# Performance work log

Measured on AMD Instinct MI355X. Metric: run time of the kernel, lower is better.

## Reference

```python
import jax, jax.numpy as jnp
import numpy as np

B, H, S, D = 2, 8, 2048, 64


def setup_inputs() -> dict:
    key = jax.random.key(0)
    kq, kk, kv, km = jax.random.split(key, 4)
    Q = jax.random.normal(kq, (B, H, S, D), dtype=jnp.float32)
    K = jax.random.normal(kk, (B, H, S, D), dtype=jnp.float32)
    V = jax.random.normal(kv, (B, H, S, D), dtype=jnp.float32)
    attn_mask = jax.random.randint(km, (B, H, S, S), 0, 2).astype(jnp.bool_)
    return {"Q": Q, "K": K, "V": V, "attn_mask": attn_mask}


def reference(Q, K, V, attn_mask):
    # a = Q K^T / sqrt(D)
    scale = 1.0 / jnp.sqrt(jnp.float32(Q.shape[-1]))
    a = jnp.einsum("bhqd,bhkd->bhqk", Q, K) * scale
    a = jnp.where(attn_mask, jnp.float32(-1e9), a)
    attn_p = jax.nn.softmax(a, axis=-1)
    # FAITHFUL to source bug: uses pre-softmax scores `a`, not attn_p
    attn_v = jnp.einsum("bhqk,bhkd->bhqd", a, V)
    return attn_v, attn_p
```

## Files before the change

kernel.cpp:

```cpp
#include <hip/hip_runtime.h>
#include <hip/hip_bf16.h>


#define SS   2048
#define DD   64
#define NT   8
#define ZMB  0
#define ZKB  4224
#define ZVB  12928
#define ZRZ  23168
#define ZAH  23296
#define MASK_B 0
#define K_B    4224
#define ARENA_H 8960
#define KST 68
#define FST 132

#define OV_F4 524288
#define ZB_F4 8192
#define PK_OFF  131072
#define PK_BYTES ((size_t)16*2048*16*16)

typedef _Float16 half4_t  __attribute__((ext_vector_type(4)));
typedef _Float16 half2_t  __attribute__((ext_vector_type(2)));
typedef short    short4_t __attribute__((ext_vector_type(4)));
typedef float    float4_t __attribute__((ext_vector_type(4)));
typedef int      int2_t   __attribute__((ext_vector_type(2)));
typedef unsigned uint2_t  __attribute__((ext_vector_type(2)));
typedef unsigned long long ulong2_t __attribute__((ext_vector_type(2)));

static __device__ __forceinline__ unsigned short f2bf_u(float f) {
  __hip_bfloat16 h = __float2bfloat16(f);
  return __builtin_bit_cast(unsigned short, h);
}
static __device__ __forceinline__ unsigned packh2(float a, float b) {
  union { half2_t h; unsigned u; } c;
  c.h.x = (_Float16)a; c.h.y = (_Float16)b;
  return c.u;
}

extern "C" __global__ __launch_bounds__(256)
void zero_k(float4_t* __restrict__ Ov, float4_t* __restrict__ Zb)
{
  const int i = blockIdx.x * 256 + threadIdx.x;
  const float4_t z = (float4_t){0.f, 0.f, 0.f, 0.f};
  if (i < OV_F4) Ov[i] = z;
  else           Zb[i - OV_F4] = z;
}

extern "C" __global__ __launch_bounds__(256, 1)
void attn_z_k(const float* __restrict__ Qg, const float* __restrict__ Kg,
              const float* __restrict__ Vg, const int* __restrict__ Mg,
              float* __restrict__ Og, float* __restrict__ Zg,
              unsigned long long* __restrict__ Wp, int do_pack)
{
  __shared__ alignas(16) unsigned short arena[ZAH];

  const int wg  = blockIdx.x;
  const int xcd = wg & 7;
  const int ii  = wg >> 3;
  const int bh  = 2 * xcd + (ii >> 9);
  const int rem = ii & 511;
  const int qg  = rem >> 2;
  const int kc  = rem & 3;

  const int tid  = threadIdx.x;
  const int w    = tid >> 6;
  const int lane = tid & 63;
  const int g    = lane >> 4;
  const int ql   = lane & 15;

  const int q0 = qg * 16;
  const int kw = kc * 512 + w * 128;

  const int srow = lane >> 4;
  const int scol = 4 * (lane & 15);

  const float* Kst = Kg + ((size_t)bh * SS + kw) * DD;
  const float* Vst = Vg + ((size_t)bh * SS + kw) * DD;

  float4_t qr[4];
  #pragma unroll
  for (int d = 0; d < 4; ++d)
    qr[d] = *(const float4_t*)(Qg + ((size_t)bh * SS + q0 + ql) * DD + 16 * d + 4 * g);

  int2_t mrow[16];
  #pragma unroll
  for (int r = 0; r < 16; ++r)
    mrow[r] = __builtin_nontemporal_load(
        (const int2_t*)(Mg + ((size_t)bh * SS + q0 + r) * SS + kw) + lane);

  float4_t kr4[4], vr4[4];
  #pragma unroll
  for (int j = 0; j < 4; ++j) {
    kr4[j] = *(const float4_t*)(Kst + (size_t)(4 * j + srow) * DD + scol);
    vr4[j] = *(const float4_t*)(Vst + (size_t)(4 * j + srow) * DD + scol);
  }

  half4_t qf[4];
  #pragma unroll
  for (int d = 0; d < 4; ++d) {
    half4_t h; h.x=(_Float16)qr[d].x; h.y=(_Float16)qr[d].y;
               h.z=(_Float16)qr[d].z; h.w=(_Float16)qr[d].w;
    qf[d] = h;
  }

  #pragma unroll
  for (int r = 0; r < 16; ++r) {
    const unsigned short pk =
        (unsigned short)((mrow[r].x ? 1u : 0u) | ((mrow[r].y ? 1u : 0u) << 8));
    arena[ZMB + w * 1056 + r * 66 + lane] = pk;
    const unsigned long long ev = __ballot(mrow[r].x != 0);
    const unsigned long long od = __ballot(mrow[r].y != 0);
    if (do_pack && lane == 0) {
      ulong2_t pm; pm.x = ev; pm.y = od;
      *(ulong2_t*)&Wp[(((size_t)bh * SS + q0 + r) * 16 + kc * 4 + w) * 2] = pm;
    }
  }

  #pragma unroll
  for (int j = 0; j < 4; ++j) {
    half4_t kh; kh.x=(_Float16)kr4[j].x; kh.y=(_Float16)kr4[j].y;
                kh.z=(_Float16)kr4[j].z; kh.w=(_Float16)kr4[j].w;
    *(half4_t*)&arena[ZKB + w * 2176 + (4 * j + srow) * 68 + scol] = kh;
    arena[ZVB + w * 2560 + (scol + 0) * 20 + 4 * j + srow] = f2bf_u(vr4[j].x);
    arena[ZVB + w * 2560 + (scol + 1) * 20 + 4 * j + srow] = f2bf_u(vr4[j].y);
    arena[ZVB + w * 2560 + (scol + 2) * 20 + 4 * j + srow] = f2bf_u(vr4[j].z);
    arena[ZVB + w * 2560 + (scol + 3) * 20 + 4 * j + srow] = f2bf_u(vr4[j].w);
  }

  float4_t accO[4];
  #pragma unroll
  for (int d = 0; d < 4; ++d) accO[d] = (float4_t){0.f, 0.f, 0.f, 0.f};
  float zs = 0.f;

  const unsigned short NEGu = 0xCE6Eu;

  #pragma unroll
  for (int t = 0; t < NT; ++t) {
    const int s = t & 1;

    if (t + 1 < NT) {
      #pragma unroll
      for (int j = 0; j < 4; ++j) {
        kr4[j] = *(const float4_t*)(Kst + (size_t)(16 * (t + 1) + 4 * j + srow) * DD + scol);
        vr4[j] = *(const float4_t*)(Vst + (size_t)(16 * (t + 1) + 4 * j + srow) * DD + scol);
      }
    }

    half4_t kf[4];
    #pragma unroll
    for (int d = 0; d < 4; ++d)
      kf[d] = *(const half4_t*)&arena[ZKB + w * 2176 + s * 1088 + ql * 68 + 16 * d + 4 * g];

    short4_t vf[4];
    #pragma unroll
    for (int d = 0; d < 4; ++d)
      vf[d] = *(const short4_t*)&arena[ZVB + w * 2560 + s * 1280 + (16 * d + ql) * 20 + 4 * g];

    const unsigned mdw = *(const unsigned*)((const unsigned char*)arena
                          + 2u * (ZMB + w * 1056 + ql * 66) + 16 * t + 4 * g);

    float4_t acc = (float4_t){0.f, 0.f, 0.f, 0.f};
    #pragma unroll
    for (int d = 0; d < 4; ++d)
      acc = __builtin_amdgcn_mfma_f32_16x16x16f16(kf[d], qf[d], acc, 0, 0, 0);

    const float a0 = (mdw & 0x000000ffu) ? -1e9f : acc.x * 0.125f;
    const float a1 = (mdw & 0x0000ff00u) ? -1e9f : acc.y * 0.125f;
    const float a2 = (mdw & 0x00ff0000u) ? -1e9f : acc.z * 0.125f;
    const float a3 = (mdw & 0xff000000u) ? -1e9f : acc.w * 0.125f;

    const float e0 = __expf(a0), e1 = __expf(a1);
    const float e2 = __expf(a2), e3 = __expf(a3);
    zs += (e0 + e1) + (e2 + e3);

    short4_t af;
    af.x = (short)((mdw & 0x000000ffu) ? NEGu : 0);
    af.y = (short)((mdw & 0x0000ff00u) ? NEGu : 0);
    af.z = (short)((mdw & 0x00ff0000u) ? NEGu : 0);
    af.w = (short)((mdw & 0xff000000u) ? NEGu : 0);
    #pragma unroll
    for (int d = 0; d < 4; ++d)
      accO[d] = __builtin_amdgcn_mfma_f32_16x16x16bf16_1k(af, vf[d], accO[d], 0, 0, 0);

    if (t + 1 < NT) {
      const int s2 = s ^ 1;
      #pragma unroll
      for (int j = 0; j < 4; ++j) {
        half4_t kh; kh.x=(_Float16)kr4[j].x; kh.y=(_Float16)kr4[j].y;
                    kh.z=(_Float16)kr4[j].z; kh.w=(_Float16)kr4[j].w;
        *(half4_t*)&arena[ZKB + w * 2176 + s2 * 1088 + (4 * j + srow) * 68 + scol] = kh;
        arena[ZVB + w * 2560 + s2 * 1280 + (scol + 0) * 20 + 4 * j + srow] = f2bf_u(vr4[j].x);
        arena[ZVB + w * 2560 + s2 * 1280 + (scol + 1) * 20 + 4 * j + srow] = f2bf_u(vr4[j].y);
        arena[ZVB + w * 2560 + s2 * 1280 + (scol + 2) * 20 + 4 * j + srow] = f2bf_u(vr4[j].z);
        arena[ZVB + w * 2560 + s2 * 1280 + (scol + 3) * 20 + 4 * j + srow] = f2bf_u(vr4[j].w);
      }
    }
  }

  zs += __shfl_xor(zs, 16);
  zs += __shfl_xor(zs, 32);
  float* redzf = (float*)&arena[ZRZ];
  if (lane < 16) redzf[w * 16 + ql] = zs;

  float* oflw = (float*)&arena[ZKB + w * 2176];
  #pragma unroll
  for (int d = 0; d < 4; ++d) {
    oflw[(4 * g + 0) * 68 + 16 * d + ql] = accO[d].x;
    oflw[(4 * g + 1) * 68 + 16 * d + ql] = accO[d].y;
    oflw[(4 * g + 2) * 68 + 16 * d + ql] = accO[d].z;
    oflw[(4 * g + 3) * 68 + 16 * d + ql] = accO[d].w;
  }
  __syncthreads();

  if (w == 0 && lane < 16) {
    const float Z = (redzf[ql] + redzf[16 + ql]) + (redzf[32 + ql] + redzf[48 + ql]);
    atomicAdd(&Zg[(size_t)bh * SS + q0 + ql], Z);
  }
  {
    const int row = tid >> 4;
    const int col = 4 * (tid & 15);
    float4_t sA = (float4_t){0.f, 0.f, 0.f, 0.f};
    #pragma unroll
    for (int W = 0; W < 4; ++W) {
      const float4_t t4 = *(const float4_t*)((const float*)&arena[ZKB + W * 2176] + row * 68 + col);
      sA.x += t4.x; sA.y += t4.y; sA.z += t4.z; sA.w += t4.w;
    }
    float* op = Og + ((size_t)bh * SS + q0 + row) * DD + col;
    atomicAdd(op + 0, sA.x);
    atomicAdd(op + 1, sA.y);
    atomicAdd(op + 2, sA.z);
    atomicAdd(op + 3, sA.w);
  }
}

extern "C" __global__ __launch_bounds__(256, 1)
void attn_p_pk(const float* __restrict__ Qg, const float* __restrict__ Kg,
               const float* __restrict__ Zg, const unsigned long long* __restrict__ Wp,
               float* __restrict__ Pg)
{
  __shared__ alignas(16) unsigned short arena[ARENA_H];

  const int wg  = blockIdx.x;
  const int xcd = wg & 7;
  const int ii  = wg >> 3;
  const int bh  = 2 * xcd + (ii >> 9);
  const int rem = ii & 511;
  const int qg  = rem >> 4;
  const int kc  = rem & 15;

  const int tid  = threadIdx.x;
  const int w    = tid >> 6;
  const int lane = tid & 63;
  const int g    = lane >> 4;
  const int ql   = lane & 15;

  const int q0 = qg * 64 + w * 16;
  const int k0 = kc * 128;

  const int krow = 4 * w + (lane >> 4);
  const int kcol = 4 * (lane & 15);

  const float* Kst = Kg + ((size_t)bh * SS + k0 + krow) * DD + kcol;

  float4_t qr[4];
  #pragma unroll
  for (int d = 0; d < 4; ++d)
    qr[d] = *(const float4_t*)(Qg + ((size_t)bh * SS + q0 + ql) * DD + 16 * d + 4 * g);

  const ulong2_t pm = *(const ulong2_t*)&Wp[(((size_t)bh * SS + q0 + ql) * 16 + kc) * 2];
  const unsigned long long ev = pm.x, od = pm.y;

  float4_t kreg = *(const float4_t*)(Kst);
  const float invZ = 1.0f / Zg[(size_t)bh * SS + q0 + ql];

  half4_t qf[4];
  #pragma unroll
  for (int d = 0; d < 4; ++d) {
    half4_t h; h.x=(_Float16)qr[d].x; h.y=(_Float16)qr[d].y;
               h.z=(_Float16)qr[d].z; h.w=(_Float16)qr[d].w;
    qf[d] = h;
  }

  {
    half4_t kh; kh.x=(_Float16)kreg.x; kh.y=(_Float16)kreg.y;
                kh.z=(_Float16)kreg.z; kh.w=(_Float16)kreg.w;
    *(half4_t*)&arena[K_B + krow * KST + kcol] = kh;
  }
  __syncthreads();

  unsigned e_dw[NT][2];

  #pragma unroll
  for (int t = 0; t < NT; ++t) {
    const int s = t & 1;

    if (t + 1 < NT)
      kreg = *(const float4_t*)(Kst + (size_t)16 * (t + 1) * DD);

    half4_t kf[4];
    #pragma unroll
    for (int d = 0; d < 4; ++d)
      kf[d] = *(const half4_t*)&arena[K_B + s * 1088 + ql * KST + 16 * d + 4 * g];

    float4_t acc = (float4_t){0.f, 0.f, 0.f, 0.f};
    #pragma unroll
    for (int d = 0; d < 4; ++d)
      acc = __builtin_amdgcn_mfma_f32_16x16x16f16(kf[d], qf[d], acc, 0, 0, 0);

    const int sh = 8 * t + 2 * g;
    const unsigned m0 = (unsigned)(ev >> sh) & 1u;
    const unsigned m1 = (unsigned)(od >> sh) & 1u;
    const unsigned m2 = (unsigned)(ev >> (sh + 1)) & 1u;
    const unsigned m3 = (unsigned)(od >> (sh + 1)) & 1u;

    const float a0 = m0 ? -1e9f : acc.x * 0.125f;
    const float a1 = m1 ? -1e9f : acc.y * 0.125f;
    const float a2 = m2 ? -1e9f : acc.z * 0.125f;
    const float a3 = m3 ? -1e9f : acc.w * 0.125f;

    const float p0 = __expf(a0) * invZ, p1 = __expf(a1) * invZ;
    const float p2 = __expf(a2) * invZ, p3 = __expf(a3) * invZ;
    e_dw[t][0] = packh2(p0, p1);
    e_dw[t][1] = packh2(p2, p3);

    if (t + 1 < NT) {
      const int s2 = s ^ 1;
      half4_t kh; kh.x=(_Float16)kreg.x; kh.y=(_Float16)kreg.y;
                  kh.z=(_Float16)kreg.z; kh.w=(_Float16)kreg.w;
      *(half4_t*)&arena[K_B + s2 * 1088 + krow * KST + kcol] = kh;
    }
    __syncthreads();
  }

  {
    unsigned short* Fw = arena + w * 2112;
    #pragma unroll
    for (int t = 0; t < NT; ++t) {
      uint2_t pk; pk.x = e_dw[t][0]; pk.y = e_dw[t][1];
      *(uint2_t*)&Fw[ql * FST + 16 * t + 4 * g] = pk;
    }
    asm volatile("s_waitcnt lgkmcnt(0)" ::: "memory");
    const size_t prow = (size_t)bh * SS + q0;
    #pragma unroll
    for (int rr = 0; rr < 8; ++rr) {
      const int row = 2 * rr + (lane >> 5);
      const half4_t ev4 = *(const half4_t*)&Fw[row * FST + 4 * (lane & 31)];
      float4_t pv;
      pv.x = (float)ev4.x; pv.y = (float)ev4.y; pv.z = (float)ev4.z; pv.w = (float)ev4.w;
      __builtin_nontemporal_store(pv, (float4_t*)(Pg + (prow + row) * SS + k0 + 4 * (lane & 31)));
    }
  }
}

extern "C" __global__ __launch_bounds__(256, 1)
void attn_p_dir(const float* __restrict__ Qg, const float* __restrict__ Kg,
                const int* __restrict__ Mg, const float* __restrict__ Zg,
                float* __restrict__ Pg)
{
  __shared__ alignas(16) unsigned short arena[ARENA_H];

  const int wg  = blockIdx.x;
  const int xcd = wg & 7;
  const int ii  = wg >> 3;
  const int bh  = 2 * xcd + (ii >> 9);
  const int rem = ii & 511;
  const int qg  = rem >> 4;
  const int kc  = rem & 15;

  const int tid  = threadIdx.x;
  const int w    = tid >> 6;
  const int lane = tid & 63;
  const int g    = lane >> 4;
  const int ql   = lane & 15;

  const int q0 = qg * 64 + w * 16;
  const int k0 = kc * 128;

  const int krow = 4 * w + (lane >> 4);
  const int kcol = 4 * (lane & 15);

  const float* Kst = Kg + ((size_t)bh * SS + k0 + krow) * DD + kcol;

  float4_t qr[4];
  #pragma unroll
  for (int d = 0; d < 4; ++d)
    qr[d] = *(const float4_t*)(Qg + ((size_t)bh * SS + q0 + ql) * DD + 16 * d + 4 * g);

  int2_t mrow[16];
  #pragma unroll
  for (int r = 0; r < 16; ++r)
    mrow[r] = *((const int2_t*)(Mg + ((size_t)bh * SS + q0 + r) * SS + k0) + lane);

  float4_t kreg = *(const float4_t*)(Kst);
  const float invZ = 1.0f / Zg[(size_t)bh * SS + q0 + ql];

  half4_t qf[4];
  #pragma unroll
  for (int d = 0; d < 4; ++d) {
    half4_t h; h.x=(_Float16)qr[d].x; h.y=(_Float16)qr[d].y;
               h.z=(_Float16)qr[d].z; h.w=(_Float16)qr[d].w;
    qf[d] = h;
  }

  #pragma unroll
  for (int r = 0; r < 16; ++r) {
    const unsigned short pk =
        (unsigned short)((mrow[r].x ? 1u : 0u) | ((mrow[r].y ? 1u : 0u) << 8));
    arena[MASK_B + w * 1056 + r * 66 + lane] = pk;
  }
  {
    half4_t kh; kh.x=(_Float16)kreg.x; kh.y=(_Float16)kreg.y;
                kh.z=(_Float16)kreg.z; kh.w=(_Float16)kreg.w;
    *(half4_t*)&arena[K_B + krow * KST + kcol] = kh;
  }
  __syncthreads();

  unsigned e_dw[NT][2];

  #pragma unroll
  for (int t = 0; t < NT; ++t) {
    const int s = t & 1;

    if (t + 1 < NT)
      kreg = *(const float4_t*)(Kst + (size_t)16 * (t + 1) * DD);

    half4_t kf[4];
    #pragma unroll
    for (int d = 0; d < 4; ++d)
      kf[d] = *(const half4_t*)&arena[K_B + s * 1088 + ql * KST + 16 * d + 4 * g];

    const unsigned mdw = *(const unsigned*)((const unsigned char*)arena
                          + 2u * (MASK_B + w * 1056 + ql * 66) + 16 * t + 4 * g);

    float4_t acc = (float4_t){0.f, 0.f, 0.f, 0.f};
    #pragma unroll
    for (int d = 0; d < 4; ++d)
      acc = __builtin_amdgcn_mfma_f32_16x16x16f16(kf[d], qf[d], acc, 0, 0, 0);

    const float a0 = (mdw & 0x000000ffu) ? -1e9f : acc.x * 0.125f;
    const float a1 = (mdw & 0x0000ff00u) ? -1e9f : acc.y * 0.125f;
    const float a2 = (mdw & 0x00ff0000u) ? -1e9f : acc.z * 0.125f;
    const float a3 = (mdw & 0xff000000u) ? -1e9f : acc.w * 0.125f;

    const float p0 = __expf(a0) * invZ, p1 = __expf(a1) * invZ;
    const float p2 = __expf(a2) * invZ, p3 = __expf(a3) * invZ;
    e_dw[t][0] = packh2(p0, p1);
    e_dw[t][1] = packh2(p2, p3);

    if (t + 1 < NT) {
      const int s2 = s ^ 1;
      half4_t kh; kh.x=(_Float16)kreg.x; kh.y=(_Float16)kreg.y;
                  kh.z=(_Float16)kreg.z; kh.w=(_Float16)kreg.w;
      *(half4_t*)&arena[K_B + s2 * 1088 + krow * KST + kcol] = kh;
    }
    __syncthreads();
  }

  {
    unsigned short* Fw = arena + w * 2112;
    #pragma unroll
    for (int t = 0; t < NT; ++t) {
      uint2_t pk; pk.x = e_dw[t][0]; pk.y = e_dw[t][1];
      *(uint2_t*)&Fw[ql * FST + 16 * t + 4 * g] = pk;
    }
    asm volatile("s_waitcnt lgkmcnt(0)" ::: "memory");
    const size_t prow = (size_t)bh * SS + q0;
    #pragma unroll
    for (int rr = 0; rr < 8; ++rr) {
      const int row = 2 * rr + (lane >> 5);
      const half4_t ev4 = *(const half4_t*)&Fw[row * FST + 4 * (lane & 31)];
      float4_t pv;
      pv.x = (float)ev4.x; pv.y = (float)ev4.y; pv.z = (float)ev4.z; pv.w = (float)ev4.w;
      __builtin_nontemporal_store(pv, (float4_t*)(Pg + (prow + row) * SS + k0 + 4 * (lane & 31)));
    }
  }
}

extern "C" void kernel_launch(void* const* d_in, const int* in_sizes, int n_in,
                              void* d_out, int out_size, void* d_ws, size_t ws_size,
                              hipStream_t stream) {
  const float* Q = (const float*)d_in[0];
  const float* K = (const float*)d_in[1];
  const float* V = (const float*)d_in[2];
  const int*   M = (const int*)d_in[3];
  float* Ov = (float*)d_out;
  float* P  = (float*)d_out + (size_t)2 * 8 * 2048 * 64;
  float* Zb = (float*)d_ws;
  unsigned long long* Wp = (unsigned long long*)((char*)d_ws + PK_OFF);
  const int packed = (ws_size >= PK_OFF + PK_BYTES) ? 1 : 0;

  zero_k<<<dim3((OV_F4 + ZB_F4) / 256), dim3(256), 0, stream>>>((float4_t*)Ov, (float4_t*)Zb);
  attn_z_k<<<dim3(8192), dim3(256), 0, stream>>>(Q, K, V, M, Ov, Zb, Wp, packed);
  if (packed)
    attn_p_pk<<<dim3(8192), dim3(256), 0, stream>>>(Q, K, Zb, Wp, P);
  else
    attn_p_dir<<<dim3(8192), dim3(256), 0, stream>>>(Q, K, M, Zb, P);
}
```

Measured before the change: 225.6 us.

## Split masked V product into separate kernel and share K tiles across waves

The Z (softmax denominator) kernel no longer computes the masked-score times V product. Its four waves now each handle different query rows and share one block-wide K tile in LDS, synchronised each step. A new attn_o kernel reads the packed mask bits (or the raw mask) plus V and computes the output per query tile, writing it directly with no atomics, so the output-zeroing pass goes away. This trades float atomics and duplicated V staging for an extra launch. The new kernel reads V uncoalesced, element by element from global memory, with a bf16 conversion on every load.

Result: faster. 180.5 us (median of 2 runs) (-20.0%).

```diff
diff --git a/kernel.cpp b/kernel.cpp
--- a/kernel.cpp
+++ b/kernel.cpp
@@ -5,18 +5,12 @@
 #define SS   2048
 #define DD   64
 #define NT   8
-#define ZMB  0
-#define ZKB  4224
-#define ZVB  12928
-#define ZRZ  23168
-#define ZAH  23296
 #define MASK_B 0
 #define K_B    4224
 #define ARENA_H 8960
 #define KST 68
 #define FST 132
 
-#define OV_F4 524288
 #define ZB_F4 8192
 #define PK_OFF  131072
 #define PK_BYTES ((size_t)16*2048*16*16)
@@ -26,6 +20,7 @@
 typedef short    short4_t __attribute__((ext_vector_type(4)));
 typedef float    float4_t __attribute__((ext_vector_type(4)));
 typedef int      int2_t   __attribute__((ext_vector_type(2)));
+typedef int      int4_t   __attribute__((ext_vector_type(4)));
 typedef unsigned uint2_t  __attribute__((ext_vector_type(2)));
 typedef unsigned long long ulong2_t __attribute__((ext_vector_type(2)));
 
@@ -40,29 +35,25 @@
 }
 
 extern "C" __global__ __launch_bounds__(256)
-void zero_k(float4_t* __restrict__ Ov, float4_t* __restrict__ Zb)
+void zero_zb(float4_t* __restrict__ Zb)
 {
-  const int i = blockIdx.x * 256 + threadIdx.x;
-  const float4_t z = (float4_t){0.f, 0.f, 0.f, 0.f};
-  if (i < OV_F4) Ov[i] = z;
-  else           Zb[i - OV_F4] = z;
+  Zb[blockIdx.x * 256 + threadIdx.x] = (float4_t){0.f, 0.f, 0.f, 0.f};
 }
 
 extern "C" __global__ __launch_bounds__(256, 1)
 void attn_z_k(const float* __restrict__ Qg, const float* __restrict__ Kg,
-              const float* __restrict__ Vg, const int* __restrict__ Mg,
-              float* __restrict__ Og, float* __restrict__ Zg,
+              const int* __restrict__ Mg, float* __restrict__ Zg,
               unsigned long long* __restrict__ Wp, int do_pack)
 {
-  __shared__ alignas(16) unsigned short arena[ZAH];
+  __shared__ alignas(16) unsigned short arena[ARENA_H];
 
   const int wg  = blockIdx.x;
   const int xcd = wg & 7;
   const int ii  = wg >> 3;
   const int bh  = 2 * xcd + (ii >> 9);
   const int rem = ii & 511;
-  const int qg  = rem >> 2;
-  const int kc  = rem & 3;
+  const int qg  = rem >> 4;
+  const int kc  = rem & 15;
 
   const int tid  = threadIdx.x;
   const int w    = tid >> 6;
@@ -70,14 +61,13 @@
   const int g    = lane >> 4;
   const int ql   = lane & 15;
 
-  const int q0 = qg * 16;
-  const int kw = kc * 512 + w * 128;
-
-  const int srow = lane >> 4;
-  const int scol = 4 * (lane & 15);
-
-  const float* Kst = Kg + ((size_t)bh * SS + kw) * DD;
-  const float* Vst = Vg + ((size_t)bh * SS + kw) * DD;
+  const int q0 = qg * 64 + w * 16;
+  const int k0 = kc * 128;
+
+  const int krow = 4 * w + (lane >> 4);
+  const int kcol = 4 * (lane & 15);
+
+  const float* Kst = Kg + ((size_t)bh * SS + k0 + krow) * DD + kcol;
 
   float4_t qr[4];
   #pragma unroll
@@ -88,14 +78,9 @@
   #pragma unroll
   for (int r = 0; r < 16; ++r)
     mrow[r] = __builtin_nontemporal_load(
-        (const int2_t*)(Mg + ((size_t)bh * SS + q0 + r) * SS + kw) + lane);
-
-  float4_t kr4[4], vr4[4];
-  #pragma unroll
-  for (int j = 0; j < 4; ++j) {
-    kr4[j] = *(const float4_t*)(Kst + (size_t)(4 * j + srow) * DD + scol);
-    vr4[j] = *(const float4_t*)(Vst + (size_t)(4 * j + srow) * DD + scol);
-  }
+        (const int2_t*)(Mg + ((size_t)bh * SS + q0 + r) * SS + k0) + lane);
+
+  float4_t kreg = *(const float4_t*)(Kst);
 
   half4_t qf[4];
   #pragma unroll
@@ -109,57 +94,38 @@
   for (int r = 0; r < 16; ++r) {
     const unsigned short pk =
         (unsigned short)((mrow[r].x ? 1u : 0u) | ((mrow[r].y ? 1u : 0u) << 8));
-    arena[ZMB + w * 1056 + r * 66 + lane] = pk;
+    arena[MASK_B + w * 1056 + r * 66 + lane] = pk;
     const unsigned long long ev = __ballot(mrow[r].x != 0);
     const unsigned long long od = __ballot(mrow[r].y != 0);
     if (do_pack && lane == 0) {
       ulong2_t pm; pm.x = ev; pm.y = od;
-      *(ulong2_t*)&Wp[(((size_t)bh * SS + q0 + r) * 16 + kc * 4 + w) * 2] = pm;
-    }
-  }
-
-  #pragma unroll
-  for (int j = 0; j < 4; ++j) {
-    half4_t kh; kh.x=(_Float16)kr4[j].x; kh.y=(_Float16)kr4[j].y;
-                kh.z=(_Float16)kr4[j].z; kh.w=(_Float16)kr4[j].w;
-    *(half4_t*)&arena[ZKB + w * 2176 + (4 * j + srow) * 68 + scol] = kh;
-    arena[ZVB + w * 2560 + (scol + 0) * 20 + 4 * j + srow] = f2bf_u(vr4[j].x);
-    arena[ZVB + w * 2560 + (scol + 1) * 20 + 4 * j + srow] = f2bf_u(vr4[j].y);
-    arena[ZVB + w * 2560 + (scol + 2) * 20 + 4 * j + srow] = f2bf_u(vr4[j].z);
-    arena[ZVB + w * 2560 + (scol + 3) * 20 + 4 * j + srow] = f2bf_u(vr4[j].w);
-  }
-
-  float4_t accO[4];
-  #pragma unroll
-  for (int d = 0; d < 4; ++d) accO[d] = (float4_t){0.f, 0.f, 0.f, 0.f};
+      *(ulong2_t*)&Wp[(((size_t)bh * SS + q0 + r) * 16 + kc) * 2] = pm;
+    }
+  }
+
+  {
+    half4_t kh; kh.x=(_Float16)kreg.x; kh.y=(_Float16)kreg.y;
+                kh.z=(_Float16)kreg.z; kh.w=(_Float16)kreg.w;
+    *(half4_t*)&arena[K_B + krow * KST + kcol] = kh;
+  }
+  __syncthreads();
+
   float zs = 0.f;
-
-  const unsigned short NEGu = 0xCE6Eu;
 
   #pragma unroll
   for (int t = 0; t < NT; ++t) {
     const int s = t & 1;
 
-    if (t + 1 < NT) {
-      #pragma unroll
-      for (int j = 0; j < 4; ++j) {
-        kr4[j] = *(const float4_t*)(Kst + (size_t)(16 * (t + 1) + 4 * j + srow) * DD + scol);
-        vr4[j] = *(const float4_t*)(Vst + (size_t)(16 * (t + 1) + 4 * j + srow) * DD + scol);
-      }
-    }
+    if (t + 1 < NT)
+      kreg = *(const float4_t*)(Kst + (size_t)16 * (t + 1) * DD);
 
     half4_t kf[4];
     #pragma unroll
     for (int d = 0; d < 4; ++d)
-      kf[d] = *(const half4_t*)&arena[ZKB + w * 2176 + s * 1088 + ql * 68 + 16 * d + 4 * g];
-
-    short4_t vf[4];
-    #pragma unroll
-    for (int d = 0; d < 4; ++d)
-      vf[d] = *(const short4_t*)&arena[ZVB + w * 2560 + s * 1280 + (16 * d + ql) * 20 + 4 * g];
+      kf[d] = *(const half4_t*)&arena[K_B + s * 1088 + ql * KST + 16 * d + 4 * g];
 
     const unsigned mdw = *(const unsigned*)((const unsigned char*)arena
-                          + 2u * (ZMB + w * 1056 + ql * 66) + 16 * t + 4 * g);
+                          + 2u * (MASK_B + w * 1056 + ql * 66) + 16 * t + 4 * g);
 
     float4_t acc = (float4_t){0.f, 0.f, 0.f, 0.f};
     #pragma unroll
@@ -175,63 +141,173 @@
     const float e2 = __expf(a2), e3 = __expf(a3);
     zs += (e0 + e1) + (e2 + e3);
 
-    short4_t af;
-    af.x = (short)((mdw & 0x000000ffu) ? NEGu : 0);
-    af.y = (short)((mdw & 0x0000ff00u) ? NEGu : 0);
-    af.z = (short)((mdw & 0x00ff0000u) ? NEGu : 0);
-    af.w = (short)((mdw & 0xff000000u) ? NEGu : 0);
-    #pragma unroll
-    for (int d = 0; d < 4; ++d)
-      accO[d] = __builtin_amdgcn_mfma_f32_16x16x16bf16_1k(af, vf[d], accO[d], 0, 0, 0);
-
     if (t + 1 < NT) {
       const int s2 = s ^ 1;
-      #pragma unroll
-      for (int j = 0; j < 4; ++j) {
-        half4_t kh; kh.x=(_Float16)kr4[j].x; kh.y=(_Float16)kr4[j].y;
-                    kh.z=(_Float16)kr4[j].z; kh.w=(_Float16)kr4[j].w;
-        *(half4_t*)&arena[ZKB + w * 2176 + s2 * 1088 + (4 * j + srow) * 68 + scol] = kh;
-        arena[ZVB + w * 2560 + s2 * 1280 + (scol + 0) * 20 + 4 * j + srow] = f2bf_u(vr4[j].x);
-        arena[ZVB + w * 2560 + s2 * 1280 + (scol + 1) * 20 + 4 * j + srow] = f2bf_u(vr4[j].y);
-        arena[ZVB + w * 2560 + s2 * 1280 + (scol + 2) * 20 + 4 * j + srow] = f2bf_u(vr4[j].z);
-        arena[ZVB + w * 2560 + s2 * 1280 + (scol + 3) * 20 + 4 * j + srow] = f2bf_u(vr4[j].w);
-      }
-    }
+      half4_t kh; kh.x=(_Float16)kreg.x; kh.y=(_Float16)kreg.y;
+                  kh.z=(_Float16)kreg.z; kh.w=(_Float16)kreg.w;
+      *(half4_t*)&arena[K_B + s2 * 1088 + krow * KST + kcol] = kh;
+    }
+    __syncthreads();
   }
 
   zs += __shfl_xor(zs, 16);
   zs += __shfl_xor(zs, 32);
-  float* redzf = (float*)&arena[ZRZ];
-  if (lane < 16) redzf[w * 16 + ql] = zs;
-
-  float* oflw = (float*)&arena[ZKB + w * 2176];
-  #pragma unroll
-  for (int d = 0; d < 4; ++d) {
-    oflw[(4 * g + 0) * 68 + 16 * d + ql] = accO[d].x;
-    oflw[(4 * g + 1) * 68 + 16 * d + ql] = accO[d].y;
-    oflw[(4 * g + 2) * 68 + 16 * d + ql] = accO[d].z;
-    oflw[(4 * g + 3) * 68 + 16 * d + ql] = accO[d].w;
+  if (lane < 16) atomicAdd(&Zg[(size_t)bh * SS + q0 + lane], zs);
+}
+
+extern "C" __global__ __launch_bounds__(256, 1)
+void attn_o_pk(const float* __restrict__ Vg, const unsigned long long* __restrict__ Wp,
+               float* __restrict__ Og)
+{
+  __shared__ float ofl[4][16][68];
+
+  const int wg  = blockIdx.x;
+  const int xcd = wg & 7;
+  const int ii  = wg >> 3;
+  const int bh  = 2 * xcd + (ii >> 7);
+  const int qg  = ii & 127;
+
+  const int tid  = threadIdx.x;
+  const int w    = tid >> 6;
+  const int lane = tid & 63;
+  const int g    = lane >> 4;
+  const int ql   = lane & 15;
+
+  const int q0 = qg * 16;
+  const float* Vb = Vg + (size_t)bh * SS * DD;
+
+  const unsigned short NEGu = 0xCE6Eu;
+
+  float4_t accO[4];
+  #pragma unroll
+  for (int d = 0; d < 4; ++d) accO[d] = (float4_t){0.f, 0.f, 0.f, 0.f};
+
+  #pragma unroll
+  for (int cc = 0; cc < 4; ++cc) {
+    const int chunk = 4 * w + cc;
+    const ulong2_t pm =
+        *(const ulong2_t*)&Wp[(((size_t)bh * SS + q0 + ql) * 16 + chunk) * 2];
+    const unsigned long long ev = pm.x, od = pm.y;
+
+    #pragma unroll
+    for (int tt = 0; tt < 8; ++tt) {
+      const int kb = chunk * 128 + 16 * tt;
+      const int sh = 8 * tt + 2 * g;
+      const unsigned m0 = (unsigned)(ev >> sh) & 1u;
+      const unsigned m1 = (unsigned)(od >> sh) & 1u;
+      const unsigned m2 = (unsigned)(ev >> (sh + 1)) & 1u;
+      const unsigned m3 = (unsigned)(od >> (sh + 1)) & 1u;
+
+      short4_t af;
+      af.x = (short)(m0 ? NEGu : 0);
+      af.y = (short)(m1 ? NEGu : 0);
+      af.z = (short)(m2 ? NEGu : 0);
+      af.w = (short)(m3 ? NEGu : 0);
+
+      #pragma unroll
+      for (int c = 0; c < 4; ++c) {
+        short4_t vf;
+        vf.x = (short)f2bf_u(Vb[(size_t)(kb + 4 * g + 0) * DD + 16 * c + ql]);
+        vf.y = (short)f2bf_u(Vb[(size_t)(kb + 4 * g + 1) * DD + 16 * c + ql]);
+        vf.z = (short)f2bf_u(Vb[(size_t)(kb + 4 * g + 2) * DD + 16 * c + ql]);
+        vf.w = (short)f2bf_u(Vb[(size_t)(kb + 4 * g + 3) * DD + 16 * c + ql]);
+        accO[c] = __builtin_amdgcn_mfma_f32_16x16x16bf16_1k(af, vf, accO[c], 0, 0, 0);
+      }
+    }
+  }
+
+  #pragma unroll
+  for (int c = 0; c < 4; ++c) {
+    ofl[w][4 * g + 0][16 * c + ql] = accO[c].x;
+    ofl[w][4 * g + 1][16 * c + ql] = accO[c].y;
+    ofl[w][4 * g + 2][16 * c + ql] = accO[c].z;
+    ofl[w][4 * g + 3][16 * c + ql] = accO[c].w;
   }
   __syncthreads();
 
-  if (w == 0 && lane < 16) {
-    const float Z = (redzf[ql] + redzf[16 + ql]) + (redzf[32 + ql] + redzf[48 + ql]);
-    atomicAdd(&Zg[(size_t)bh * SS + q0 + ql], Z);
-  }
   {
     const int row = tid >> 4;
     const int col = 4 * (tid & 15);
     float4_t sA = (float4_t){0.f, 0.f, 0.f, 0.f};
     #pragma unroll
     for (int W = 0; W < 4; ++W) {
-      const float4_t t4 = *(const float4_t*)((const float*)&arena[ZKB + W * 2176] + row * 68 + col);
+      const float4_t t4 = *(const float4_t*)&ofl[W][row][col];
       sA.x += t4.x; sA.y += t4.y; sA.z += t4.z; sA.w += t4.w;
     }
-    float* op = Og + ((size_t)bh * SS + q0 + row) * DD + col;
-    atomicAdd(op + 0, sA.x);
-    atomicAdd(op + 1, sA.y);
-    atomicAdd(op + 2, sA.z);
-    atomicAdd(op + 3, sA.w);
+    *(float4_t*)(Og + ((size_t)bh * SS + q0 + row) * DD + col) = sA;
+  }
+}
+
+extern "C" __global__ __launch_bounds__(256, 1)
+void attn_o_dir(const float* __restrict__ Vg, const int* __restrict__ Mg,
+                float* __restrict__ Og)
+{
+  __shared__ float ofl[4][16][68];
+
+  const int wg  = blockIdx.x;
+  const int xcd = wg & 7;
+  const int ii  = wg >> 3;
+  const int bh  = 2 * xcd + (ii >> 7);
+  const int qg  = ii & 127;
+
+  const int tid  = threadIdx.x;
+  const int w    = tid >> 6;
+  const int lane = tid & 63;
+  const int g    = lane >> 4;
+  const int ql   = lane & 15;
+
+  const int q0 = qg * 16;
+  const float* Vb = Vg + (size_t)bh * SS * DD;
+  const int*   Mb = Mg + ((size_t)bh * SS + q0 + ql) * SS;
+
+  const unsigned short NEGu = 0xCE6Eu;
+
+  float4_t accO[4];
+  #pragma unroll
+  for (int d = 0; d < 4; ++d) accO[d] = (float4_t){0.f, 0.f, 0.f, 0.f};
+
+  #pragma unroll
+  for (int cc = 0; cc < 4; ++cc) {
+    #pragma unroll
+    for (int tt = 0; tt < 8; ++tt) {
+      const int kb = (4 * w + cc) * 128 + 16 * tt;
+      const int4_t m4 = *(const int4_t*)(Mb + kb + 4 * g);
+      short4_t af;
+      af.x = (short)(m4.x ? NEGu : 0);
+      af.y = (short)(m4.y ? NEGu : 0);
+      af.z = (short)(m4.z ? NEGu : 0);
+      af.w = (short)(m4.w ? NEGu : 0);
+      #pragma unroll
+      for (int c = 0; c < 4; ++c) {
+        short4_t vf;
+        vf.x = (short)f2bf_u(Vb[(size_t)(kb + 4 * g + 0) * DD + 16 * c + ql]);
+        vf.y = (short)f2bf_u(Vb[(size_t)(kb + 4 * g + 1) * DD + 16 * c + ql]);
+        vf.z = (short)f2bf_u(Vb[(size_t)(kb + 4 * g + 2) * DD + 16 * c + ql]);
+        vf.w = (short)f2bf_u(Vb[(size_t)(kb + 4 * g + 3) * DD + 16 * c + ql]);
+        accO[c] = __builtin_amdgcn_mfma_f32_16x16x16bf16_1k(af, vf, accO[c], 0, 0, 0);
+      }
+    }
+  }
+
+  #pragma unroll
+  for (int c = 0; c < 4; ++c) {
+    ofl[w][4 * g + 0][16 * c + ql] = accO[c].x;
+    ofl[w][4 * g + 1][16 * c + ql] = accO[c].y;
+    ofl[w][4 * g + 2][16 * c + ql] = accO[c].z;
+    ofl[w][4 * g + 3][16 * c + ql] = accO[c].w;
+  }
+  __syncthreads();
+
+  {
+    const int row = tid >> 4;
+    const int col = 4 * (tid & 15);
+    float4_t sA = (float4_t){0.f, 0.f, 0.f, 0.f};
+    #pragma unroll
+    for (int W = 0; W < 4; ++W) {
+      const float4_t t4 = *(const float4_t*)&ofl[W][row][col];
+      sA.x += t4.x; sA.y += t4.y; sA.z += t4.z; sA.w += t4.w;
+    }
+    *(float4_t*)(Og + ((size_t)bh * SS + q0 + row) * DD + col) = sA;
   }
 }
 
@@ -491,10 +567,13 @@
   unsigned long long* Wp = (unsigned long long*)((char*)d_ws + PK_OFF);
   const int packed = (ws_size >= PK_OFF + PK_BYTES) ? 1 : 0;
 
-  zero_k<<<dim3((OV_F4 + ZB_F4) / 256), dim3(256), 0, stream>>>((float4_t*)Ov, (float4_t*)Zb);
-  attn_z_k<<<dim3(8192), dim3(256), 0, stream>>>(Q, K, V, M, Ov, Zb, Wp, packed);
-  if (packed)
+  zero_zb<<<dim3(ZB_F4 / 256), dim3(256), 0, stream>>>((float4_t*)Zb);
+  attn_z_k<<<dim3(8192), dim3(256), 0, stream>>>(Q, K, M, Zb, Wp, packed);
+  if (packed) {
+    attn_o_pk<<<dim3(2048), dim3(256), 0, stream>>>(V, Wp, Ov);
     attn_p_pk<<<dim3(8192), dim3(256), 0, stream>>>(Q, K, Zb, Wp, P);
-  else
+  } else {
+    attn_o_dir<<<dim3(2048), dim3(256), 0, stream>>>(V, M, Ov);
     attn_p_dir<<<dim3(8192), dim3(256), 0, stream>>>(Q, K, M, Zb, P);
-}
+  }
+}
```
